# Optimization experiments

Measured on AMD Instinct MI355X. Metric: run time of the kernel, lower is better.

The kernel has to match this reference:

```python
import jax, jax.numpy as jnp
import numpy as np

HEADS = 8
LN_EPS = 1e-5


def _elu_plus_one(t):
    # F.elu(x) + 1 == exp(x) for x<0, x+1 for x>=0
    return jax.nn.elu(t) + 1.0


def setup_inputs() -> dict:
    key = jax.random.key(0)
    k1, k2, k3 = jax.random.split(key, 3)
    dim = 256
    x = jax.random.normal(k1, (16, dim, 64, 64), dtype=jnp.float32)
    w_qkv = jax.random.normal(k2, (3 * dim, dim), dtype=jnp.float32) * 0.02
    w_out = jax.random.normal(k3, (dim, dim), dtype=jnp.float32) * 0.02
    ln_gamma = jnp.ones((dim,), dtype=jnp.float32)
    ln_beta = jnp.zeros((dim,), dtype=jnp.float32)
    return {"x": x, "w_qkv": w_qkv, "w_out": w_out, "ln_gamma": ln_gamma, "ln_beta": ln_beta}


def reference(x, w_qkv, w_out, ln_gamma, ln_beta):
    b, c, h, w = x.shape
    hd = c // HEADS
    n = h * w
    # 1x1 conv == per-pixel matmul over channels
    qkv = jnp.einsum('bchw,oc->bohw', x, w_qkv)  # [b, 3c, h, w]
    q, k, v = jnp.split(qkv, 3, axis=1)
    q = q.reshape(b, HEADS, hd, n)
    k = k.reshape(b, HEADS, hd, n)
    v = v.reshape(b, HEADS, hd, n)
    qk = _elu_plus_one(q)
    kk = _elu_plus_one(k)
    # channel-wise kv reduction over spatial positions (NOT an outer product)
    kv = jnp.sum(kk * v, axis=-1, keepdims=True)        # [b, heads, hd, 1]
    denom = jnp.maximum(jnp.sum(kk, axis=-1, keepdims=True), 1e-6)
    out = qk * (kv / denom)                              # [b, heads, hd, n]
    out = out.reshape(b, c, h, w)
    out = jnp.einsum('bchw,oc->bohw', out, w_out)        # 1x1 output conv
    # LayerNorm over channel dim (module permutes to NHWC first)
    t = jnp.transpose(out, (0, 2, 3, 1))                 # [b, h, w, c]
    mu = jnp.mean(t, axis=-1, keepdims=True)
    var = jnp.mean(jnp.square(t - mu), axis=-1, keepdims=True)
    t = (t - mu) * jax.lax.rsqrt(var + LN_EPS) * ln_gamma + ln_beta
    return jnp.transpose(t, (0, 3, 1, 2))
```

## Files before the change

kernel.cpp:

```cpp
#include <hip/hip_runtime.h>


#define NB 16
#define NC 256
#define NN 4096
#define LN_EPS 1e-5f
#define IOSCALE (1.0f/1024.0f)

typedef _Float16 f16;
typedef _Float16 f16x8 __attribute__((ext_vector_type(8)));
typedef _Float16 f16x4v __attribute__((ext_vector_type(4)));
typedef float f32x4 __attribute__((ext_vector_type(4)));

typedef __attribute__((address_space(1))) const unsigned int* as1cu32;
typedef __attribute__((address_space(3))) unsigned int* as3u32;

__device__ __forceinline__ void gload16(const void* g, void* l) {
  __builtin_amdgcn_global_load_lds((as1cu32)g, (as3u32)l, 16, 0, 0);
}
__device__ __forceinline__ float elu1(float x) {
  return x > 0.f ? x + 1.f : __expf(x);
}
#define MFMA16 __builtin_amdgcn_mfma_f32_16x16x32_f16

__global__ __launch_bounds__(256) void k_init(const float* __restrict__ wqkv,
                                              const float* __restrict__ wout,
                                              f16* __restrict__ wh,
                                              f16* __restrict__ wouth,
                                              float* __restrict__ kvden) {
  int i = blockIdx.x * 256 + threadIdx.x;
  wh[i] = (f16)wqkv[i];
  if (i < 65536) wouth[i] = (f16)wout[i];
  if (i < 8192) kvden[i] = 0.f;
}

__global__ __launch_bounds__(256) void k_transpose(const float* __restrict__ x,
                                                   f16* __restrict__ xh) {
  __shared__ float t[64 * 65];
  const int b = blockIdx.z, c0 = blockIdx.y * 64, n0 = blockIdx.x * 64;
  const int tid = threadIdx.x;
#pragma unroll
  for (int i = 0; i < 4; ++i) {
    int lin = tid + i * 256;
    int r = lin >> 4;
    int cg = lin & 15;
    const float4 v = *reinterpret_cast<const float4*>(
        &x[((size_t)(b * NC + c0 + r)) * NN + n0 + cg * 4]);
    t[r * 65 + cg * 4 + 0] = v.x;
    t[r * 65 + cg * 4 + 1] = v.y;
    t[r * 65 + cg * 4 + 2] = v.z;
    t[r * 65 + cg * 4 + 3] = v.w;
  }
  __syncthreads();
#pragma unroll
  for (int i = 0; i < 4; ++i) {
    int lin = tid + i * 256;
    int nr = lin >> 4;
    int cg = lin & 15;
    f16x4v h;
    h[0] = (f16)t[(cg * 4 + 0) * 65 + nr];
    h[1] = (f16)t[(cg * 4 + 1) * 65 + nr];
    h[2] = (f16)t[(cg * 4 + 2) * 65 + nr];
    h[3] = (f16)t[(cg * 4 + 3) * 65 + nr];
    *reinterpret_cast<f16x4v*>(&xh[((size_t)(b * NN + n0 + nr)) * NC + c0 + cg * 4]) = h;
  }
}

__global__ __launch_bounds__(1024, 4) void k_kv(const f16* __restrict__ xh,
                                                const f16* __restrict__ wh,
                                                float* __restrict__ kv,
                                                float* __restrict__ den) {
  __shared__ __align__(16) f16 Xt[128 * 256];
  __shared__ __align__(16) f16 Bt[2][512 * 32];
  const int b = blockIdx.y;
  const int n0 = blockIdx.x * 128;
  const int tid = threadIdx.x;
  const int lane = tid & 63;
  const int wv = tid >> 6;
  const int ng = wv >> 2, cg = wv & 3;
  const int l15 = lane & 15, lg = lane >> 4;

  {
    const int rsub = lane >> 5;
    const int u = lane & 31;
#pragma unroll
    for (int i = 0; i < 4; ++i) {
      const int inst = wv * 4 + i;
      const int row = inst * 2 + rsub;
      gload16(xh + ((size_t)(b * NN + n0 + row)) * NC + ((u ^ (row & 31)) * 8),
              &Xt[inst * 512]);
    }
  }

  auto stageB = [&](int s, int bb) {
    const int c0 = s * 32;
    const int rsub = lane >> 2;
    const int u = lane & 3;
#pragma unroll
    for (int i = 0; i < 2; ++i) {
      const int inst = wv * 2 + i;
      const int row = inst * 16 + rsub;
      gload16(wh + (size_t)(256 + row) * NC + c0 + ((u ^ ((row >> 1) & 3)) * 8),
              &Bt[bb][inst * 512]);
    }
  };

  stageB(0, 0);
  __syncthreads();

  f32x4 kacc[2][4] = {};
  f32x4 vacc[2][4] = {};
  for (int s = 0; s < 8; ++s) {
    const int cb = s & 1;
    if (s < 7) stageB(s + 1, cb ^ 1);
    f16x8 a[2];
#pragma unroll
    for (int m = 0; m < 2; ++m) {
      const int R = ng * 32 + m * 16 + l15;
      const int U = s * 4 + lg;
      a[m] = *(const f16x8*)(&Xt[R * 256 + ((U ^ (R & 31)) * 8)]);
    }
#pragma unroll
    for (int f = 0; f < 4; ++f) {
      const int Rk = cg * 64 + f * 16 + l15;
      const f16x8 bk = *(const f16x8*)(&Bt[cb][Rk * 32 + ((lg ^ ((Rk >> 1) & 3)) * 8)]);
      const int Rv = 256 + Rk;
      const f16x8 bv = *(const f16x8*)(&Bt[cb][Rv * 32 + ((lg ^ ((Rv >> 1) & 3)) * 8)]);
#pragma unroll
      for (int m = 0; m < 2; ++m) {
        kacc[m][f] = MFMA16(a[m], bk, kacc[m][f], 0, 0, 0);
        vacc[m][f] = MFMA16(a[m], bv, vacc[m][f], 0, 0, 0);
      }
    }
    if (s < 7) __syncthreads();
  }

  float pkv[4] = {0.f, 0.f, 0.f, 0.f}, pden[4] = {0.f, 0.f, 0.f, 0.f};
#pragma unroll
  for (int f = 0; f < 4; ++f)
#pragma unroll
    for (int m = 0; m < 2; ++m)
#pragma unroll
      for (int j = 0; j < 4; ++j) {
        const float kk = elu1(kacc[m][f][j]);
        pkv[f] += kk * vacc[m][f][j];
        pden[f] += kk;
      }
#pragma unroll
  for (int f = 0; f < 4; ++f) {
    pkv[f] += __shfl_xor(pkv[f], 16, 64);
    pkv[f] += __shfl_xor(pkv[f], 32, 64);
    pden[f] += __shfl_xor(pden[f], 16, 64);
    pden[f] += __shfl_xor(pden[f], 32, 64);
  }
  if (lane < 16) {
#pragma unroll
    for (int f = 0; f < 4; ++f) {
      const int c = cg * 64 + f * 16 + lane;
      atomicAdd(&kv[b * NC + c], pkv[f]);
      atomicAdd(&den[b * NC + c], pden[f]);
    }
  }
}

__global__ __launch_bounds__(1024, 4) void k_fused2(const f16* __restrict__ xh,
                                                    const f16* __restrict__ wh,
                                                    const f16* __restrict__ wouth,
                                                    const float* __restrict__ kv,
                                                    const float* __restrict__ den,
                                                    const float* __restrict__ gamma,
                                                    const float* __restrict__ beta,
                                                    float* __restrict__ out) {
  __shared__ __align__(16) f16 XQ[128 * 256];
  __shared__ __align__(16) f16 Wt[2][256 * 32];
  __shared__ float s1024[256];
  const int b = blockIdx.y;
  const int n0 = blockIdx.x * 128;
  const int tid = threadIdx.x;
  const int lane = tid & 63;
  const int wv = tid >> 6;
  const int cg = wv & 3, ng = wv >> 2;
  const int l15 = lane & 15, lg = lane >> 4;

  {
    const int rsub = lane >> 5;
    const int u = lane & 31;
#pragma unroll
    for (int i = 0; i < 4; ++i) {
      const int inst = wv * 4 + i;
      const int row = inst * 2 + rsub;
      gload16(xh + ((size_t)(b * NN + n0 + row)) * NC + ((u ^ (row & 31)) * 8),
              &XQ[inst * 512]);
    }
  }
  if (tid < 256)
    s1024[tid] = kv[b * NC + tid] / fmaxf(den[b * NC + tid], 1e-6f) * 1024.0f;

  auto stageW = [&](const f16* __restrict__ W, int s, int bb) {
    const int c0 = s * 32;
    const int row = wv * 16 + (lane >> 2);
    const int u = lane & 3;
    gload16(W + (size_t)row * NC + c0 + ((u ^ ((row >> 1) & 3)) * 8),
            &Wt[bb][wv * 512]);
  };

  stageW(wh, 0, 0);
  __syncthreads();

  f32x4 acc[4][2] = {};
  for (int s = 0; s < 8; ++s) {
    const int cb = s & 1;
    if (s < 7) stageW(wh, s + 1, cb ^ 1);
    else stageW(wouth, 0, cb ^ 1);
    f16x8 a[4], bx[2];
#pragma unroll
    for (int m = 0; m < 4; ++m) {
      const int R = cg * 64 + m * 16 + l15;
      a[m] = *(const f16x8*)(&Wt[cb][R * 32 + ((lg ^ ((R >> 1) & 3)) * 8)]);
    }
#pragma unroll
    for (int f = 0; f < 2; ++f) {
      const int Rn = ng * 32 + f * 16 + l15;
      const int U = s * 4 + lg;
      bx[f] = *(const f16x8*)(&XQ[Rn * 256 + ((U ^ (Rn & 31)) * 8)]);
    }
#pragma unroll
    for (int m = 0; m < 4; ++m)
#pragma unroll
      for (int f = 0; f < 2; ++f)
        acc[m][f] = MFMA16(a[m], bx[f], acc[m][f], 0, 0, 0);
    __syncthreads();
  }

#pragma unroll
  for (int m = 0; m < 4; ++m) {
    const int ch = cg * 64 + m * 16 + lg * 4;
    const float4 sv = *reinterpret_cast<const float4*>(&s1024[ch]);
    const int u = ch >> 3;
#pragma unroll
    for (int f = 0; f < 2; ++f) {
      const int n = ng * 32 + f * 16 + l15;
      f16x4v h;
      h[0] = (f16)(elu1(acc[m][f][0]) * sv.x);
      h[1] = (f16)(elu1(acc[m][f][1]) * sv.y);
      h[2] = (f16)(elu1(acc[m][f][2]) * sv.z);
      h[3] = (f16)(elu1(acc[m][f][3]) * sv.w);
      *reinterpret_cast<f16x4v*>(&XQ[n * 256 + ((u ^ (n & 31)) * 8) + (ch & 7)]) = h;
    }
  }
  __syncthreads();

  f32x4 acc2[4][2] = {};
  for (int s = 0; s < 8; ++s) {
    const int cb = s & 1;
    if (s < 7) stageW(wouth, s + 1, cb ^ 1);
    f16x8 a[4], bq[2];
#pragma unroll
    for (int m = 0; m < 4; ++m) {
      const int R = cg * 64 + m * 16 + l15;
      a[m] = *(const f16x8*)(&Wt[cb][R * 32 + ((lg ^ ((R >> 1) & 3)) * 8)]);
    }
#pragma unroll
    for (int f = 0; f < 2; ++f) {
      const int n = ng * 32 + f * 16 + l15;
      const int U = s * 4 + lg;
      bq[f] = *(const f16x8*)(&XQ[n * 256 + ((U ^ (n & 31)) * 8)]);
    }
#pragma unroll
    for (int m = 0; m < 4; ++m)
#pragma unroll
      for (int f = 0; f < 2; ++f)
        acc2[m][f] = MFMA16(a[m], bq[f], acc2[m][f], 0, 0, 0);
    if (s < 7) __syncthreads();
  }

  float* red1 = (float*)(&Wt[0][0]);
  float* red2 = red1 + 512;
  float* smu = red2 + 512;
  float* srs = smu + 128;
  float s1[2] = {0, 0}, s2[2] = {0, 0};
#pragma unroll
  for (int f = 0; f < 2; ++f)
#pragma unroll
    for (int m = 0; m < 4; ++m)
#pragma unroll
      for (int j = 0; j < 4; ++j) {
        const float v = acc2[m][f][j];
        s1[f] += v;
        s2[f] += v * v;
      }
#pragma unroll
  for (int f = 0; f < 2; ++f) {
    s1[f] += __shfl_xor(s1[f], 16, 64);
    s1[f] += __shfl_xor(s1[f], 32, 64);
    s2[f] += __shfl_xor(s2[f], 16, 64);
    s2[f] += __shfl_xor(s2[f], 32, 64);
  }
  __syncthreads();
  if (lane < 16) {
#pragma unroll
    for (int f = 0; f < 2; ++f) {
      const int col = ng * 32 + f * 16 + lane;
      red1[cg * 128 + col] = s1[f];
      red2[cg * 128 + col] = s2[f];
    }
  }
  __syncthreads();
  if (tid < 128) {
    const float a1 = red1[tid] + red1[128 + tid] + red1[256 + tid] + red1[384 + tid];
    const float a2 = red2[tid] + red2[128 + tid] + red2[256 + tid] + red2[384 + tid];
    const float mu = a1 * (IOSCALE / 256.f);
    const float e2 = a2 * (IOSCALE * IOSCALE / 256.f);
    smu[tid] = mu;
    srs[tid] = rsqrtf(e2 - mu * mu + LN_EPS);
  }
  __syncthreads();
#pragma unroll
  for (int m = 0; m < 4; ++m) {
    const int ob = cg * 64 + m * 16 + lg * 4;
#pragma unroll
    for (int j = 0; j < 4; ++j) {
      const int o = ob + j;
      const float g = gamma[o], be = beta[o];
#pragma unroll
      for (int f = 0; f < 2; ++f) {
        const int col = ng * 32 + f * 16 + l15;
        const float v = acc2[m][f][j] * IOSCALE;
        out[((size_t)(b * NC + o)) * NN + n0 + col] = (v - smu[col]) * srs[col] * g + be;
      }
    }
  }
}

extern "C" void kernel_launch(void* const* d_in, const int* in_sizes, int n_in,
                              void* d_out, int out_size, void* d_ws, size_t ws_size,
                              hipStream_t stream) {
  const float* x = (const float*)d_in[0];
  const float* w_qkv = (const float*)d_in[1];
  const float* w_out = (const float*)d_in[2];
  const float* ln_g = (const float*)d_in[3];
  const float* ln_b = (const float*)d_in[4];
  float* out = (float*)d_out;

  char* wsb = (char*)d_ws;
  const size_t OFF_WH = 0;
  const size_t OFF_WOUTH = 393216;
  const size_t OFF_XH = OFF_WOUTH + 131072;
  const size_t OFF_KV = OFF_XH + 33554432;
  const size_t OFF_DEN = OFF_KV + 16384;

  f16* wh = (f16*)(wsb + OFF_WH);
  f16* wouth = (f16*)(wsb + OFF_WOUTH);
  f16* xh = (f16*)(wsb + OFF_XH);
  float* kv = (float*)(wsb + OFF_KV);
  float* den = (float*)(wsb + OFF_DEN);

  k_init<<<768, 256, 0, stream>>>(w_qkv, w_out, wh, wouth, kv);
  k_transpose<<<dim3(64, 4, 16), 256, 0, stream>>>(x, xh);
  k_kv<<<dim3(32, 16), 1024, 0, stream>>>(xh, wh, kv, den);
  k_fused2<<<dim3(32, 16), 1024, 0, stream>>>(xh, wh, wouth, kv, den, ln_g, ln_b, out);
}
```

Baseline: 87.76 us.

## Halve fused kernel block to 512 threads with larger per-wave tiles and K-steps

Reworks the fused GEMM/LN kernel to use 8 waves of 512 threads, each computing a 64x64 tile (4x4 MFMA) instead of 64x32. The weight stage now covers 64 channels per step, so there are 4 K-steps instead of 8, with a new XOR swizzle. The kv/den scale is held in registers rather than shared memory. The aim is more register-level data reuse and fewer barriers, at the cost of higher register pressure and fewer waves for latency hiding.

Result: no change. 88.90 us (+1.3%).

```diff
diff --git a/kernel.cpp b/kernel.cpp
--- a/kernel.cpp
+++ b/kernel.cpp
@@ -163,124 +163,141 @@
   }
 }
 
-__global__ __launch_bounds__(1024, 4) void k_fused2(const f16* __restrict__ xh,
-                                                    const f16* __restrict__ wh,
-                                                    const f16* __restrict__ wouth,
-                                                    const float* __restrict__ kv,
-                                                    const float* __restrict__ den,
-                                                    const float* __restrict__ gamma,
-                                                    const float* __restrict__ beta,
-                                                    float* __restrict__ out) {
+__global__ __launch_bounds__(512, 1) void k_fused2(const f16* __restrict__ xh,
+                                                   const f16* __restrict__ wh,
+                                                   const f16* __restrict__ wouth,
+                                                   const float* __restrict__ kv,
+                                                   const float* __restrict__ den,
+                                                   const float* __restrict__ gamma,
+                                                   const float* __restrict__ beta,
+                                                   float* __restrict__ out) {
   __shared__ __align__(16) f16 XQ[128 * 256];
-  __shared__ __align__(16) f16 Wt[2][256 * 32];
-  __shared__ float s1024[256];
+  __shared__ __align__(16) f16 Wt[2][256 * 64];
   const int b = blockIdx.y;
   const int n0 = blockIdx.x * 128;
   const int tid = threadIdx.x;
   const int lane = tid & 63;
   const int wv = tid >> 6;
-  const int cg = wv & 3, ng = wv >> 2;
+  const int cg = wv >> 1, ng = wv & 1;
   const int l15 = lane & 15, lg = lane >> 4;
 
   {
     const int rsub = lane >> 5;
     const int u = lane & 31;
 #pragma unroll
-    for (int i = 0; i < 4; ++i) {
-      const int inst = wv * 4 + i;
+    for (int i = 0; i < 8; ++i) {
+      const int inst = wv * 8 + i;
       const int row = inst * 2 + rsub;
       gload16(xh + ((size_t)(b * NN + n0 + row)) * NC + ((u ^ (row & 31)) * 8),
               &XQ[inst * 512]);
     }
   }
-  if (tid < 256)
-    s1024[tid] = kv[b * NC + tid] / fmaxf(den[b * NC + tid], 1e-6f) * 1024.0f;
-
+
+  float sreg[4][4];
+#pragma unroll
+  for (int m = 0; m < 4; ++m)
+#pragma unroll
+    for (int j = 0; j < 4; ++j) {
+      const int c = cg * 64 + m * 16 + lg * 4 + j;
+      sreg[m][j] = kv[b * NC + c] / fmaxf(den[b * NC + c], 1e-6f) * 1024.0f;
+    }
+
+  const int lr8 = lane >> 3;
+  const int sw = ((lane & 7) ^ lr8) * 8;
   auto stageW = [&](const f16* __restrict__ W, int s, int bb) {
-    const int c0 = s * 32;
-    const int row = wv * 16 + (lane >> 2);
-    const int u = lane & 3;
-    gload16(W + (size_t)row * NC + c0 + ((u ^ ((row >> 1) & 3)) * 8),
-            &Wt[bb][wv * 512]);
+    const int c0 = s * 64;
+#pragma unroll
+    for (int i = 0; i < 4; ++i) {
+      const int inst = wv * 4 + i;
+      const int row = inst * 8 + lr8;
+      gload16(W + (size_t)row * NC + c0 + sw, &Wt[bb][inst * 512]);
+    }
   };
 
   stageW(wh, 0, 0);
   __syncthreads();
 
-  f32x4 acc[4][2] = {};
-  for (int s = 0; s < 8; ++s) {
+  f32x4 acc[4][4] = {};
+  for (int s = 0; s < 4; ++s) {
     const int cb = s & 1;
-    if (s < 7) stageW(wh, s + 1, cb ^ 1);
+    if (s < 3) stageW(wh, s + 1, cb ^ 1);
     else stageW(wouth, 0, cb ^ 1);
-    f16x8 a[4], bx[2];
-#pragma unroll
-    for (int m = 0; m < 4; ++m) {
-      const int R = cg * 64 + m * 16 + l15;
-      a[m] = *(const f16x8*)(&Wt[cb][R * 32 + ((lg ^ ((R >> 1) & 3)) * 8)]);
-    }
-#pragma unroll
-    for (int f = 0; f < 2; ++f) {
-      const int Rn = ng * 32 + f * 16 + l15;
-      const int U = s * 4 + lg;
-      bx[f] = *(const f16x8*)(&XQ[Rn * 256 + ((U ^ (Rn & 31)) * 8)]);
-    }
-#pragma unroll
-    for (int m = 0; m < 4; ++m)
-#pragma unroll
-      for (int f = 0; f < 2; ++f)
-        acc[m][f] = MFMA16(a[m], bx[f], acc[m][f], 0, 0, 0);
+#pragma unroll
+    for (int kk = 0; kk < 2; ++kk) {
+      f16x8 a[4], bx[4];
+#pragma unroll
+      for (int m = 0; m < 4; ++m) {
+        const int R = cg * 64 + m * 16 + l15;
+        const int U = kk * 4 + lg;
+        a[m] = *(const f16x8*)(&Wt[cb][R * 64 + ((U ^ (R & 7)) << 3)]);
+      }
+#pragma unroll
+      for (int f = 0; f < 4; ++f) {
+        const int Rn = ng * 64 + f * 16 + l15;
+        const int U = s * 8 + kk * 4 + lg;
+        bx[f] = *(const f16x8*)(&XQ[Rn * 256 + ((U ^ (Rn & 31)) << 3)]);
+      }
+#pragma unroll
+      for (int m = 0; m < 4; ++m)
+#pragma unroll
+        for (int f = 0; f < 4; ++f)
+          acc[m][f] = MFMA16(a[m], bx[f], acc[m][f], 0, 0, 0);
+    }
     __syncthreads();
   }
 
 #pragma unroll
   for (int m = 0; m < 4; ++m) {
     const int ch = cg * 64 + m * 16 + lg * 4;
-    const float4 sv = *reinterpret_cast<const float4*>(&s1024[ch]);
     const int u = ch >> 3;
 #pragma unroll
-    for (int f = 0; f < 2; ++f) {
-      const int n = ng * 32 + f * 16 + l15;
+    for (int f = 0; f < 4; ++f) {
+      const int n = ng * 64 + f * 16 + l15;
       f16x4v h;
-      h[0] = (f16)(elu1(acc[m][f][0]) * sv.x);
-      h[1] = (f16)(elu1(acc[m][f][1]) * sv.y);
-      h[2] = (f16)(elu1(acc[m][f][2]) * sv.z);
-      h[3] = (f16)(elu1(acc[m][f][3]) * sv.w);
-      *reinterpret_cast<f16x4v*>(&XQ[n * 256 + ((u ^ (n & 31)) * 8) + (ch & 7)]) = h;
-    }
-  }
-  __syncthreads();
-
-  f32x4 acc2[4][2] = {};
-  for (int s = 0; s < 8; ++s) {
+      h[0] = (f16)(elu1(acc[m][f][0]) * sreg[m][0]);
+      h[1] = (f16)(elu1(acc[m][f][1]) * sreg[m][1]);
+      h[2] = (f16)(elu1(acc[m][f][2]) * sreg[m][2]);
+      h[3] = (f16)(elu1(acc[m][f][3]) * sreg[m][3]);
+      *reinterpret_cast<f16x4v*>(&XQ[n * 256 + ((u ^ (n & 31)) << 3) + (ch & 7)]) = h;
+    }
+  }
+  __syncthreads();
+
+  f32x4 acc2[4][4] = {};
+  for (int s = 0; s < 4; ++s) {
     const int cb = s & 1;
-    if (s < 7) stageW(wouth, s + 1, cb ^ 1);
-    f16x8 a[4], bq[2];
-#pragma unroll
-    for (int m = 0; m < 4; ++m) {
-      const int R = cg * 64 + m * 16 + l15;
-      a[m] = *(const f16x8*)(&Wt[cb][R * 32 + ((lg ^ ((R >> 1) & 3)) * 8)]);
-    }
-#pragma unroll
-    for (int f = 0; f < 2; ++f) {
-      const int n = ng * 32 + f * 16 + l15;
-      const int U = s * 4 + lg;
-      bq[f] = *(const f16x8*)(&XQ[n * 256 + ((U ^ (n & 31)) * 8)]);
-    }
-#pragma unroll
-    for (int m = 0; m < 4; ++m)
-#pragma unroll
-      for (int f = 0; f < 2; ++f)
-        acc2[m][f] = MFMA16(a[m], bq[f], acc2[m][f], 0, 0, 0);
-    if (s < 7) __syncthreads();
+    if (s < 3) stageW(wouth, s + 1, cb ^ 1);
+#pragma unroll
+    for (int kk = 0; kk < 2; ++kk) {
+      f16x8 a[4], bq[4];
+#pragma unroll
+      for (int m = 0; m < 4; ++m) {
+        const int R = cg * 64 + m * 16 + l15;
+        const int U = kk * 4 + lg;
+        a[m] = *(const f16x8*)(&Wt[cb][R * 64 + ((U ^ (R & 7)) << 3)]);
+      }
+#pragma unroll
+      for (int f = 0; f < 4; ++f) {
+        const int n = ng * 64 + f * 16 + l15;
+        const int U = s * 8 + kk * 4 + lg;
+        bq[f] = *(const f16x8*)(&XQ[n * 256 + ((U ^ (n & 31)) << 3)]);
+      }
+#pragma unroll
+      for (int m = 0; m < 4; ++m)
+#pragma unroll
+        for (int f = 0; f < 4; ++f)
+          acc2[m][f] = MFMA16(a[m], bq[f], acc2[m][f], 0, 0, 0);
+    }
+    __syncthreads();
   }
 
   float* red1 = (float*)(&Wt[0][0]);
   float* red2 = red1 + 512;
   float* smu = red2 + 512;
   float* srs = smu + 128;
-  float s1[2] = {0, 0}, s2[2] = {0, 0};
-#pragma unroll
-  for (int f = 0; f < 2; ++f)
+  float s1[4] = {0, 0, 0, 0}, s2[4] = {0, 0, 0, 0};
+#pragma unroll
+  for (int f = 0; f < 4; ++f)
 #pragma unroll
     for (int m = 0; m < 4; ++m)
 #pragma unroll
@@ -290,17 +307,16 @@
         s2[f] += v * v;
       }
 #pragma unroll
-  for (int f = 0; f < 2; ++f) {
+  for (int f = 0; f < 4; ++f) {
     s1[f] += __shfl_xor(s1[f], 16, 64);
     s1[f] += __shfl_xor(s1[f], 32, 64);
     s2[f] += __shfl_xor(s2[f], 16, 64);
     s2[f] += __shfl_xor(s2[f], 32, 64);
   }
-  __syncthreads();
   if (lane < 16) {
 #pragma unroll
-    for (int f = 0; f < 2; ++f) {
-      const int col = ng * 32 + f * 16 + lane;
+    for (int f = 0; f < 4; ++f) {
+      const int col = ng * 64 + f * 16 + lane;
       red1[cg * 128 + col] = s1[f];
       red2[cg * 128 + col] = s2[f];
     }
@@ -323,8 +339,8 @@
       const int o = ob + j;
       const float g = gamma[o], be = beta[o];
 #pragma unroll
-      for (int f = 0; f < 2; ++f) {
-        const int col = ng * 32 + f * 16 + l15;
+      for (int f = 0; f < 4; ++f) {
+        const int col = ng * 64 + f * 16 + l15;
         const float v = acc2[m][f][j] * IOSCALE;
         out[((size_t)(b * NC + o)) * NN + n0 + col] = (v - smu[col]) * srs[col] * g + be;
       }
@@ -358,5 +374,5 @@
   k_init<<<768, 256, 0, stream>>>(w_qkv, w_out, wh, wouth, kv);
   k_transpose<<<dim3(64, 4, 16), 256, 0, stream>>>(x, xh);
   k_kv<<<dim3(32, 16), 1024, 0, stream>>>(xh, wh, kv, den);
-  k_fused2<<<dim3(32, 16), 1024, 0, stream>>>(xh, wh, wouth, kv, den, ln_g, ln_b, out);
-}
+  k_fused2<<<dim3(32, 16), 512, 0, stream>>>(xh, wh, wouth, kv, den, ln_g, ln_b, out);
+}
```
